# Kernel tuning notes

Hardware: AMD Instinct MI355X
Metric: run time of the kernel (lower is better)

## Reference

```python
import jax, jax.numpy as jnp
import numpy as np

N = 16384          # num_nodes
B = 2              # batch_size
F = 32             # feature_size (hard-coded in module)
G = 16             # num_gru_units
OUT = 16           # output_dim


def _normalized_laplacian(adj):
    # calculate_laplacian_with_self_loop: D^-1/2 (A + I) D^-1/2
    a = adj + jnp.eye(adj.shape[0], dtype=adj.dtype)
    d = a.sum(axis=1)
    dinv = jax.lax.rsqrt(d)
    return dinv[:, None] * a * dinv[None, :]


def setup_inputs() -> dict:
    key = jax.random.key(0)
    k1, k2, k3, k4 = jax.random.split(key, 4)
    adj = (jax.random.uniform(k1, (N, N), dtype=jnp.float32) < 0.01).astype(jnp.float32)
    laplacian = _normalized_laplacian(adj)
    inputs = jax.random.normal(k2, (B, N, F), dtype=jnp.float32)
    hidden_state = jax.random.normal(k3, (B, N * G), dtype=jnp.float32)
    # xavier_uniform for weights [(G+F), OUT]
    limit = np.sqrt(6.0 / (G + F + OUT)).astype(np.float32)
    weights = jax.random.uniform(k4, (G + F, OUT), dtype=jnp.float32, minval=-limit, maxval=limit)
    biases = jnp.zeros((OUT,), dtype=jnp.float32)
    return {"inputs": inputs, "hidden_state": hidden_state, "laplacian": laplacian,
            "weights": weights, "biases": biases}


def reference(inputs, hidden_state, laplacian, weights, biases):
    b, n, f = inputs.shape
    g = weights.shape[0] - f
    out_dim = weights.shape[1]
    h = hidden_state.reshape(b, n, g)
    cat = jnp.concatenate([inputs, h], axis=2)              # [B, N, F+G]
    # laplacian @ concat over the node dimension (same math as the
    # reshape/transpose dance + per-batch sparse GEMM loop in the original)
    ax = jnp.einsum('mn,bnc->bmc', laplacian, cat)          # [B, N, F+G]
    out = ax @ weights + biases                             # [B, N, OUT]
    return out.reshape(b, n * out_dim)
```

## Files before the change

### kernel.cpp

```cpp
#include <hip/hip_runtime.h>
#include <hip/hip_bf16.h>


#define NN   16384
#define FF   32
#define GG   16
#define OUTD 16
#define C96  96

__device__ __forceinline__ unsigned int pack_bf2(float lo, float hi) {
  unsigned short a = __builtin_bit_cast(unsigned short, __float2bfloat16(lo));
  unsigned short b = __builtin_bit_cast(unsigned short, __float2bfloat16(hi));
  return (unsigned int)a | ((unsigned int)b << 16);
}

__global__ __launch_bounds__(256) void prep_xp(const float* __restrict__ inp,
                                               const float* __restrict__ hid,
                                               unsigned int* __restrict__ xpb) {
  int gid = blockIdx.x * 256 + threadIdx.x;
  int k = gid / 12;
  int j = gid - k * 12;
  const float* src;
  if (j < 4)       src = inp + (size_t)k * FF + 8 * j;
  else if (j < 6)  src = hid + (size_t)k * GG + 8 * (j - 4);
  else if (j < 10) src = inp + ((size_t)NN + k) * FF + 8 * (j - 6);
  else             src = hid + ((size_t)NN + k) * GG + 8 * (j - 10);
  float4 v0 = *(const float4*)src;
  float4 v1 = *(const float4*)(src + 4);
  uint4 o;
  o.x = pack_bf2(v0.x, v0.y);
  o.y = pack_bf2(v0.z, v0.w);
  o.z = pack_bf2(v1.x, v1.y);
  o.w = pack_bf2(v1.z, v1.w);
  ((uint4*)xpb)[gid] = o;
}

__global__ __launch_bounds__(256) void spmm_sparse(const float* __restrict__ L,
                                                   const unsigned int* __restrict__ xpb,
                                                   float* __restrict__ crow) {
  const int lane = threadIdx.x & 63;
  const int wave = threadIdx.x >> 6;
  const int cl = lane < 48 ? lane : lane - 48;

#pragma unroll
  for (int r = 0; r < 2; ++r) {
    const int m = blockIdx.x * 8 + wave * 2 + r;
    const float4* lrow = (const float4*)(L + (size_t)m * NN);
    float accx = 0.f, accy = 0.f;

    int idx = lane * 2;
    float4 c0 = lrow[idx];
    float4 c1 = lrow[idx + 1];

    for (int step = 0; step < 32; ++step) {
      int nidx = (step < 31) ? idx + 128 : lane * 2;
      float4 n0 = lrow[nidx];
      float4 n1 = lrow[nidx + 1];
      const int kstep = step * 512;

#pragma unroll
      for (int s = 0; s < 8; ++s) {
        float v;
        switch (s) {
          case 0: v = c0.x; break; case 1: v = c0.y; break;
          case 2: v = c0.z; break; case 3: v = c0.w; break;
          case 4: v = c1.x; break; case 5: v = c1.y; break;
          case 6: v = c1.z; break; default: v = c1.w; break;
        }
        unsigned long long msk = __ballot(v != 0.0f);
        while (msk) {
          int b = __builtin_ctzll(msk);
          msk &= msk - 1;
          float val = __shfl(v, b);
          int k = kstep + 8 * b + s;
          unsigned int u = xpb[(size_t)k * 48 + cl];
          float x0 = __builtin_bit_cast(float, u << 16);
          float x1 = __builtin_bit_cast(float, u & 0xffff0000u);
          accx += val * x0;
          accy += val * x1;
        }
      }
      c0 = n0; c1 = n1; idx = nidx;
    }

    if (lane < 48) {
      float2 o = {accx, accy};
      *(float2*)(crow + (size_t)m * C96 + 2 * lane) = o;
    }
  }
}

__global__ __launch_bounds__(256) void epilogue(const float* __restrict__ cp,
                                                const float* __restrict__ w,
                                                const float* __restrict__ bias,
                                                float* __restrict__ out) {
  __shared__ float lds_c[64 * 97];
  __shared__ float lds_w[48 * 16];
  __shared__ float lds_bias[16];
  const int tid = threadIdx.x;
  const int n0 = blockIdx.x * 64;

  for (int i = tid; i < 768; i += 256) lds_w[i] = w[i];
  if (tid < 16) lds_bias[tid] = bias[tid];

  const size_t base = (size_t)n0 * C96;
#pragma unroll
  for (int i = 0; i < 24; ++i) {
    int e = tid + i * 256;
    lds_c[e + e / 96] = cp[base + e];
  }
  __syncthreads();

  const int node = tid >> 2;
  const int b = (tid >> 1) & 1;
  const int o0 = (tid & 1) * 8;
  const float* crow_l = &lds_c[node * 97 + b * 48];
  float accv[8];
#pragma unroll
  for (int o = 0; o < 8; ++o) accv[o] = lds_bias[o0 + o];
#pragma unroll
  for (int j = 0; j < 48; ++j) {
    float cv = crow_l[j];
#pragma unroll
    for (int o = 0; o < 8; ++o) accv[o] += cv * lds_w[j * 16 + o0 + o];
  }
  size_t ob = (size_t)b * ((size_t)NN * OUTD) + (size_t)(n0 + node) * OUTD + o0;
  float4 v0 = {accv[0], accv[1], accv[2], accv[3]};
  float4 v1 = {accv[4], accv[5], accv[6], accv[7]};
  *(float4*)(out + ob) = v0;
  *(float4*)(out + ob + 4) = v1;
}

extern "C" void kernel_launch(void* const* d_in, const int* in_sizes, int n_in,
                              void* d_out, int out_size, void* d_ws, size_t ws_size,
                              hipStream_t stream) {
  (void)in_sizes; (void)n_in; (void)out_size; (void)ws_size;
  const float* inp = (const float*)d_in[0];
  const float* hid = (const float*)d_in[1];
  const float* lap = (const float*)d_in[2];
  const float* wts = (const float*)d_in[3];
  const float* bia = (const float*)d_in[4];
  float* out = (float*)d_out;

  unsigned int* xpb = (unsigned int*)d_ws;
  float* crow = (float*)((char*)d_ws + (4u << 20));

  prep_xp<<<(NN * 12) / 256, 256, 0, stream>>>(inp, hid, xpb);
  spmm_sparse<<<NN / 8, 256, 0, stream>>>(lap, xpb, crow);
  epilogue<<<NN / 64, 256, 0, stream>>>(crow, wts, bia, out);
}
```

Measured before the change: 1.376 ms.

## Compress Laplacian rows into nonzero lists, then gather in a separate kernel

Splits the fused dense-scan plus sparse-gather kernel into two passes. The first pass streams each Laplacian row and writes compacted (index, value) lists padded to multiples of 64. The second pass walks those lists with an unrolled broadcast loop so many gathers of the packed features can be in flight at once. This removes the serialized ballot/ctz loop from the bandwidth-bound scan, at the cost of writing and reading an extra list buffer and relying on a fixed 512-slot cap per row.

```diff
diff --git a/kernel.cpp b/kernel.cpp
--- a/kernel.cpp
+++ b/kernel.cpp
@@ -7,6 +7,7 @@
 #define GG   16
 #define OUTD 16
 #define C96  96
+#define NSTRIDE 512
 
 __device__ __forceinline__ unsigned int pack_bf2(float lo, float hi) {
   unsigned short a = __builtin_bit_cast(unsigned short, __float2bfloat16(lo));
@@ -35,58 +36,70 @@
   ((uint4*)xpb)[gid] = o;
 }
 
-__global__ __launch_bounds__(256) void spmm_sparse(const float* __restrict__ L,
+__global__ __launch_bounds__(256) void compress_l(const float* __restrict__ L,
+                                                  uint2* __restrict__ lists,
+                                                  unsigned int* __restrict__ counts) {
+  const int lane = threadIdx.x & 63;
+  const int wave = threadIdx.x >> 6;
+  const int m = blockIdx.x * 4 + wave;
+  const float4* lrow4 = (const float4*)(L + (size_t)m * NN);
+  uint2* rowlist = lists + (size_t)m * NSTRIDE;
+  const unsigned long long below = (1ull << lane) - 1ull;
+  unsigned int cnt = 0;
+
+  for (int g = 0; g < 16; ++g) {
+    float4 v[4];
+#pragma unroll
+    for (int c = 0; c < 4; ++c) v[c] = lrow4[(g * 4 + c) * 64 + lane];
+#pragma unroll
+    for (int c = 0; c < 4; ++c) {
+      const int kb = (g * 4 + c) * 256 + lane * 4;
+#pragma unroll
+      for (int e = 0; e < 4; ++e) {
+        float x = (e == 0) ? v[c].x : (e == 1) ? v[c].y : (e == 2) ? v[c].z : v[c].w;
+        unsigned long long msk = __ballot(x != 0.0f);
+        if (x != 0.0f) {
+          unsigned int pos = cnt + (unsigned)__popcll(msk & below);
+          rowlist[pos] = make_uint2((unsigned)(kb + e),
+                                    __builtin_bit_cast(unsigned int, x));
+        }
+        cnt += (unsigned)__popcll(msk);
+      }
+    }
+  }
+  unsigned int pad = (64u - (cnt & 63u)) & 63u;
+  if ((unsigned)lane < pad) rowlist[cnt + lane] = make_uint2(0u, 0u);
+  cnt += pad;
+  if (lane == 0) counts[m] = cnt;
+}
+
+__global__ __launch_bounds__(256) void spmm_gather(const uint2* __restrict__ lists,
+                                                   const unsigned int* __restrict__ counts,
                                                    const unsigned int* __restrict__ xpb,
                                                    float* __restrict__ crow) {
   const int lane = threadIdx.x & 63;
   const int wave = threadIdx.x >> 6;
+  const int m = blockIdx.x * 4 + wave;
   const int cl = lane < 48 ? lane : lane - 48;
+  const uint2* rowlist = lists + (size_t)m * NSTRIDE;
+  const unsigned int cnt = counts[m];
+  float accx = 0.f, accy = 0.f;
 
-#pragma unroll
-  for (int r = 0; r < 2; ++r) {
-    const int m = blockIdx.x * 8 + wave * 2 + r;
-    const float4* lrow = (const float4*)(L + (size_t)m * NN);
-    float accx = 0.f, accy = 0.f;
+  for (unsigned int b = 0; b < cnt; b += 64) {
+    uint2 kv = rowlist[b + lane];
+#pragma unroll 16
+    for (int j = 0; j < 64; ++j) {
+      unsigned int k = (unsigned int)__shfl((int)kv.x, j);
+      float val = __builtin_bit_cast(float, (unsigned int)__shfl((int)kv.y, j));
+      unsigned int u = xpb[(size_t)k * 48 + cl];
+      accx += val * __builtin_bit_cast(float, u << 16);
+      accy += val * __builtin_bit_cast(float, u & 0xffff0000u);
+    }
+  }
 
-    int idx = lane * 2;
-    float4 c0 = lrow[idx];
-    float4 c1 = lrow[idx + 1];
-
-    for (int step = 0; step < 32; ++step) {
-      int nidx = (step < 31) ? idx + 128 : lane * 2;
-      float4 n0 = lrow[nidx];
-      float4 n1 = lrow[nidx + 1];
-      const int kstep = step * 512;
-
-#pragma unroll
-      for (int s = 0; s < 8; ++s) {
-        float v;
-        switch (s) {
-          case 0: v = c0.x; break; case 1: v = c0.y; break;
-          case 2: v = c0.z; break; case 3: v = c0.w; break;
-          case 4: v = c1.x; break; case 5: v = c1.y; break;
-          case 6: v = c1.z; break; default: v = c1.w; break;
-        }
-        unsigned long long msk = __ballot(v != 0.0f);
-        while (msk) {
-          int b = __builtin_ctzll(msk);
-          msk &= msk - 1;
-          float val = __shfl(v, b);
-          int k = kstep + 8 * b + s;
-          unsigned int u = xpb[(size_t)k * 48 + cl];
-          float x0 = __builtin_bit_cast(float, u << 16);
-          float x1 = __builtin_bit_cast(float, u & 0xffff0000u);
-          accx += val * x0;
-          accy += val * x1;
-        }
-      }
-      c0 = n0; c1 = n1; idx = nidx;
-    }
-
-    if (lane < 48) {
-      float2 o = {accx, accy};
-      *(float2*)(crow + (size_t)m * C96 + 2 * lane) = o;
-    }
+  if (lane < 48) {
+    float2 o = {accx, accy};
+    *(float2*)(crow + (size_t)m * C96 + 2 * lane) = o;
   }
 }
 
@@ -144,8 +157,11 @@
 
   unsigned int* xpb = (unsigned int*)d_ws;
   float* crow = (float*)((char*)d_ws + (4u << 20));
+  uint2* lists = (uint2*)((char*)d_ws + (16u << 20));
+  unsigned int* counts = (unsigned int*)((char*)d_ws + (96u << 20));
 
   prep_xp<<<(NN * 12) / 256, 256, 0, stream>>>(inp, hid, xpb);
-  spmm_sparse<<<NN / 8, 256, 0, stream>>>(lap, xpb, crow);
+  compress_l<<<NN / 4, 256, 0, stream>>>(lap, lists, counts);
+  spmm_gather<<<NN / 4, 256, 0, stream>>>(lists, counts, xpb, crow);
   epilogue<<<NN / 64, 256, 0, stream>>>(crow, wts, bia, out);
 }
```

Result: slower. 1.456 ms (+5.8%).
